# Kernel optimization log

Hardware: AMD Instinct MI355X
Metric: run time of the kernel (lower is better)

Reference implementation:

```python
import jax, jax.numpy as jnp
import numpy as np

EPS = 1e-12

def _dot(x, y):
    return jnp.sum(x * y, axis=-1)

def _safe(x):
    # avoid div-by-zero for degenerate triangles / unused where-branches
    return jnp.where(jnp.abs(x) < EPS, EPS, x)

def _closest_point_on_tri(p, a, b, c):
    """Ericson real-time-collision-detection closest point on triangle.
    p: [B,Q,1,3]; a,b,c: [B,1,F,3]. Returns [B,Q,F,3]."""
    ab = b - a
    ac = c - a
    ap = p - a
    d1 = _dot(ab, ap)
    d2 = _dot(ac, ap)
    bp = p - b
    d3 = _dot(ab, bp)
    d4 = _dot(ac, bp)
    cp = p - c
    d5 = _dot(ab, cp)
    d6 = _dot(ac, cp)
    vc = d1 * d4 - d3 * d2
    vb = d5 * d2 - d1 * d6
    va = d3 * d6 - d5 * d4
    # candidate points (all computed densely, selected by masks)
    t_ab = (d1 / _safe(d1 - d3))[..., None]
    t_ac = (d2 / _safe(d2 - d6))[..., None]
    t_bc = ((d4 - d3) / _safe((d4 - d3) + (d5 - d6)))[..., None]
    denom = _safe(va + vb + vc)
    v = (vb / denom)[..., None]
    w = (vc / denom)[..., None]
    res = a + ab * v + ac * w  # face interior
    cond_bc = ((va <= 0) & ((d4 - d3) >= 0) & ((d5 - d6) >= 0))[..., None]
    cond_ac = ((vb <= 0) & (d2 >= 0) & (d6 <= 0))[..., None]
    cond_c = ((d6 >= 0) & (d5 <= d6))[..., None]
    cond_ab = ((vc <= 0) & (d1 >= 0) & (d3 <= 0))[..., None]
    cond_b = ((d3 >= 0) & (d4 <= d3))[..., None]
    cond_a = ((d1 <= 0) & (d2 <= 0))[..., None]
    res = jnp.where(cond_bc, b + (c - b) * t_bc, res)
    res = jnp.where(cond_ac, a + ac * t_ac, res)
    res = jnp.where(cond_c, c, res)
    res = jnp.where(cond_ab, a + ab * t_ab, res)
    res = jnp.where(cond_b, b, res)
    res = jnp.where(cond_a, a, res)
    return res

def setup_inputs() -> dict:
    key = jax.random.key(0)
    k1, k2, k3 = jax.random.split(key, 3)
    B, nQ, nV, nF = 1, 8192, 1024, 2048
    vertices = jax.random.normal(k1, (B, nV, 3), dtype=jnp.float32)
    query = jax.random.normal(k2, (B, nQ, 3), dtype=jnp.float32)
    faces = jax.random.randint(k3, (nF, 3), 0, nV, dtype=jnp.int32)
    return {"faces": faces, "vertices": vertices, "query": query}

def reference(faces, vertices, query):
    # gather triangle vertices: [B, F, 3(verts), 3(xyz)]
    tri = vertices[:, faces, :]
    a = tri[:, :, 0][:, None]  # [B,1,F,3]
    b = tri[:, :, 1][:, None]
    c = tri[:, :, 2][:, None]
    p = query[:, :, None, :]   # [B,Q,1,3]
    cp = _closest_point_on_tri(p, a, b, c)        # [B,Q,F,3]
    d2 = jnp.sum((p - cp) ** 2, axis=-1)          # [B,Q,F]
    idx = jnp.argmin(d2, axis=-1)                 # [B,Q]
    B_, Q_ = idx.shape
    cp_best = jnp.take_along_axis(
        cp, jnp.broadcast_to(idx[:, :, None, None], (B_, Q_, 1, 3)), axis=2
    )[:, :, 0]                                    # [B,Q,3]
    d2_best = jnp.take_along_axis(d2, idx[:, :, None], axis=2)[:, :, 0]
    # face normals for sign (outside if along normal), per-face then gathered
    n = jnp.cross(tri[:, :, 1] - tri[:, :, 0], tri[:, :, 2] - tri[:, :, 0])  # [B,F,3]
    n_best = jnp.take_along_axis(n, jnp.broadcast_to(idx[:, :, None], (B_, Q_, 3)) % n.shape[1] * 0 + idx[:, :, None], axis=1)  # [B,Q,3]
    sign = jnp.where(jnp.sum((query - cp_best) * n_best, axis=-1) >= 0, 1.0, -1.0)
    sdist = sign * jnp.sqrt(jnp.maximum(d2_best, 0.0))
    phi = jnp.concatenate([cp_best, sdist[..., None]], axis=-1)  # [B,Q,4]
    return phi
```

## Files before the change

kernel.cpp:

```cpp
#include <hip/hip_runtime.h>
#include <stdint.h>


#define QPB 256
#define FC  64
#define RECF 20

__device__ __forceinline__ float safe32(float x) {
    return (fabsf(x) < 1e-12f) ? 1e-12f : x;
}

__device__ __forceinline__ float cp32(
    float px, float py, float pz, const float4* __restrict__ rec,
    float& rx, float& ry, float& rz)
{
#pragma clang fp contract(off)
    float4 r0 = rec[0], r1 = rec[1], r2 = rec[2], r3 = rec[3], r4 = rec[4];
    float ax = r0.x, ay = r0.y, az = r0.z, bx = r0.w;
    float by = r1.x, bz = r1.y, cx = r1.z, cy = r1.w;
    float cz = r2.x, abx = r2.y, aby = r2.z, abz = r2.w;
    float acx = r3.x, acy = r3.y, acz = r3.z, cbx = r3.w;
    float cby = r4.x, cbz = r4.y;

    float apx = px - ax, apy = py - ay, apz = pz - az;
    float bpx = px - bx, bpy = py - by, bpz = pz - bz;
    float qpx = px - cx, qpy = py - cy, qpz = pz - cz;

    float d1 = ((abx * apx) + (aby * apy)) + (abz * apz);
    float d2 = ((acx * apx) + (acy * apy)) + (acz * apz);
    float d3 = ((abx * bpx) + (aby * bpy)) + (abz * bpz);
    float d4 = ((acx * bpx) + (acy * bpy)) + (acz * bpz);
    float d5 = ((abx * qpx) + (aby * qpy)) + (abz * qpz);
    float d6 = ((acx * qpx) + (acy * qpy)) + (acz * qpz);

    float vc = (d1 * d4) - (d3 * d2);
    float vb = (d5 * d2) - (d1 * d6);
    float va = (d3 * d6) - (d5 * d4);
    float e1 = d4 - d3;
    float e2 = d5 - d6;

    bool ca  = (d1 <= 0.0f) && (d2 <= 0.0f);
    bool cb_ = (d3 >= 0.0f) && (d4 <= d3);
    bool cab = (vc <= 0.0f) && (d1 >= 0.0f) && (d3 <= 0.0f);
    bool cc  = (d6 >= 0.0f) && (d5 <= d6);
    bool cac = (vb <= 0.0f) && (d2 >= 0.0f) && (d6 <= 0.0f);
    bool cbc = (va <= 0.0f) && (e1 >= 0.0f) && (e2 >= 0.0f);

    bool tk  = ca;
    bool m_b  = cb_ && !tk;  tk = tk || cb_;
    bool m_ab = cab && !tk;  tk = tk || cab;
    bool m_c  = cc  && !tk;  tk = tk || cc;
    bool m_ac = cac && !tk;  tk = tk || cac;
    bool m_bc = cbc && !tk;  tk = tk || cbc;
    bool m_in = !tk;

    float denom_raw = (va + vb) + vc;
    float num1 = m_ab ? d1 : m_ac ? d2 : m_bc ? e1 : m_in ? vb : 0.0f;
    float den1_raw = m_ab ? (d1 - d3) : m_ac ? (d2 - d6)
                   : m_bc ? (e1 + e2) : m_in ? denom_raw : 1.0f;
    float den1  = safe32(den1_raw);
    float denom = safe32(denom_raw);
    float num2  = m_in ? vc : 0.0f;
    float q1 = num1 / den1;
    float q2 = num2 / denom;

    bool sel_b = m_b || m_bc;
    float basx = m_c ? cx : sel_b ? bx : ax;
    float basy = m_c ? cy : sel_b ? by : ay;
    float basz = m_c ? cz : sel_b ? bz : az;

    bool s_ab = m_ab || m_in;
    float t1x = m_bc ? cbx : m_ac ? acx : s_ab ? abx : 0.0f;
    float t1y = m_bc ? cby : m_ac ? acy : s_ab ? aby : 0.0f;
    float t1z = m_bc ? cbz : m_ac ? acz : s_ab ? abz : 0.0f;

    float t2x = m_in ? acx : 0.0f;
    float t2y = m_in ? acy : 0.0f;
    float t2z = m_in ? acz : 0.0f;

    rx = (basx + (t1x * q1)) + (t2x * q2);
    ry = (basy + (t1y * q1)) + (t2y * q2);
    rz = (basz + (t1z * q1)) + (t2z * q2);

    float dx = px - rx, dy = py - ry, dz = pz - rz;
    return ((dx * dx) + (dy * dy)) + (dz * dz);
}

__global__ void k_prep(const int* __restrict__ faces, const float* __restrict__ verts,
                       float* __restrict__ tris, unsigned long long* __restrict__ keys,
                       int nF, int nQ)
{
#pragma clang fp contract(off)
    int i = blockIdx.x * 256 + threadIdx.x;
    if (i < nQ) keys[i] = 0xffffffffffffffffULL;
    if (i < nF) {
        int i0 = faces[i * 3 + 0], i1 = faces[i * 3 + 1], i2 = faces[i * 3 + 2];
        float ax = verts[i0 * 3], ay = verts[i0 * 3 + 1], az = verts[i0 * 3 + 2];
        float bx = verts[i1 * 3], by = verts[i1 * 3 + 1], bz = verts[i1 * 3 + 2];
        float cx = verts[i2 * 3], cy = verts[i2 * 3 + 1], cz = verts[i2 * 3 + 2];
        float* t = &tris[i * RECF];
        t[0]  = ax; t[1]  = ay; t[2]  = az; t[3]  = bx;
        t[4]  = by; t[5]  = bz; t[6]  = cx; t[7]  = cy;
        t[8]  = cz;
        t[9]  = bx - ax; t[10] = by - ay; t[11] = bz - az;
        t[12] = cx - ax; t[13] = cy - ay; t[14] = cz - az;
        t[15] = cx - bx; t[16] = cy - by; t[17] = cz - bz;
        t[18] = 0.0f; t[19] = 0.0f;
    }
}

__global__ __launch_bounds__(QPB) void k_main(
    const float* __restrict__ tris, const float* __restrict__ query,
    unsigned long long* __restrict__ keys, int nF, int nQ)
{
    __shared__ float4 s4[FC * (RECF / 4)];
    const int fbase = blockIdx.y * FC;
    const int nf = min(FC, nF - fbase);
    const int tid = threadIdx.x;

    {
        const float4* src = (const float4*)&tris[(size_t)fbase * RECF];
        for (int i = tid; i < nf * (RECF / 4); i += QPB) s4[i] = src[i];
    }
    __syncthreads();

    const int q = blockIdx.x * QPB + tid;
    if (q >= nQ) return;
    const float px = query[q * 3], py = query[q * 3 + 1], pz = query[q * 3 + 2];

    float best = 3.402823466e38f;
    int bidx = 0x7fffffff;
    for (int f = 0; f < nf; ++f) {
        float rx, ry, rz;
        float d2 = cp32(px, py, pz, &s4[f * (RECF / 4)], rx, ry, rz);
        if (d2 < best) { best = d2; bidx = fbase + f; }
    }
    unsigned long long key =
        ((unsigned long long)__float_as_uint(best) << 32) | (unsigned)bidx;
    atomicMin(&keys[q], key);
}

__global__ void k_final(const float* __restrict__ tris, const float* __restrict__ query,
                        const unsigned long long* __restrict__ keys,
                        float* __restrict__ out, int nQ)
{
#pragma clang fp contract(off)
    int q = blockIdx.x * 256 + threadIdx.x;
    if (q >= nQ) return;
    unsigned long long key = keys[q];
    unsigned idx = (unsigned)(key & 0xffffffffu);
    float best_d2 = __uint_as_float((unsigned)(key >> 32));

    const float px = query[q * 3], py = query[q * 3 + 1], pz = query[q * 3 + 2];
    const float4* rec = (const float4*)&tris[(size_t)idx * RECF];
    float rx, ry, rz;
    cp32(px, py, pz, rec, rx, ry, rz);

    float4 r2 = rec[2], r3 = rec[3];
    float abx = r2.y, aby = r2.z, abz = r2.w;
    float acx = r3.x, acy = r3.y, acz = r3.z;
    float nx = (aby * acz) - (abz * acy);
    float ny = (abz * acx) - (abx * acz);
    float nz = (abx * acy) - (aby * acx);

    float dx = px - rx, dy = py - ry, dz = pz - rz;
    float sdot = ((dx * nx) + (dy * ny)) + (dz * nz);
    float sgn = (sdot >= 0.0f) ? 1.0f : -1.0f;
    float sdist = sgn * __fsqrt_rn(fmaxf(best_d2, 0.0f));

    out[q * 4 + 0] = rx;
    out[q * 4 + 1] = ry;
    out[q * 4 + 2] = rz;
    out[q * 4 + 3] = sdist;
}

extern "C" void kernel_launch(void* const* d_in, const int* in_sizes, int n_in,
                              void* d_out, int out_size, void* d_ws, size_t ws_size,
                              hipStream_t stream) {
    const int* faces = (const int*)d_in[0];
    const float* verts = (const float*)d_in[1];
    const float* query = (const float*)d_in[2];
    float* out = (float*)d_out;

    const int nF = in_sizes[0] / 3;
    const int nQ = in_sizes[2] / 3;

    unsigned long long* keys = (unsigned long long*)d_ws;
    float* tris = (float*)((char*)d_ws + (size_t)nQ * 8);

    int prep_threads = (nQ > nF ? nQ : nF);
    k_prep<<<(prep_threads + 255) / 256, 256, 0, stream>>>(faces, verts, tris, keys, nF, nQ);

    dim3 grid((nQ + QPB - 1) / QPB, (nF + FC - 1) / FC);
    k_main<<<grid, QPB, 0, stream>>>(tris, query, keys, nF, nQ);

    k_final<<<(nQ + 255) / 256, 256, 0, stream>>>(tris, query, keys, out, nQ);
}
```

Before: 127.2 us.

## Read triangle records directly from global memory instead of LDS staging

Drops the shared-memory staging of triangle records and the block barrier, so each thread reads the records straight from global memory. Every thread in a block reads the same address, so the compiler can turn these into uniform scalar loads. It also halves the faces per block, which doubles the grid and the atomicMin traffic on the keys, and adds a 2x unroll. The risk is that scalar-cache loads with no staging add latency, and that the extra atomics cost more than the removed sync saves.

```diff
diff --git a/kernel.cpp b/kernel.cpp
--- a/kernel.cpp
+++ b/kernel.cpp
@@ -3,7 +3,7 @@
 
 
 #define QPB 256
-#define FC  64
+#define FC  32
 #define RECF 20
 
 __device__ __forceinline__ float safe32(float x) {
@@ -11,16 +11,16 @@
 }
 
 __device__ __forceinline__ float cp32(
-    float px, float py, float pz, const float4* __restrict__ rec,
+    float px, float py, float pz, const float* __restrict__ t,
     float& rx, float& ry, float& rz)
 {
 #pragma clang fp contract(off)
-    float4 r0 = rec[0], r1 = rec[1], r2 = rec[2], r3 = rec[3], r4 = rec[4];
-    float ax = r0.x, ay = r0.y, az = r0.z, bx = r0.w;
-    float by = r1.x, bz = r1.y, cx = r1.z, cy = r1.w;
-    float cz = r2.x, abx = r2.y, aby = r2.z, abz = r2.w;
-    float acx = r3.x, acy = r3.y, acz = r3.z, cbx = r3.w;
-    float cby = r4.x, cbz = r4.y;
+    float ax  = t[0],  ay  = t[1],  az  = t[2];
+    float bx  = t[3],  by  = t[4],  bz  = t[5];
+    float cx  = t[6],  cy  = t[7],  cz  = t[8];
+    float abx = t[9],  aby = t[10], abz = t[11];
+    float acx = t[12], acy = t[13], acz = t[14];
+    float cbx = t[15], cby = t[16], cbz = t[17];
 
     float apx = px - ax, apy = py - ay, apz = pz - az;
     float bpx = px - bx, bpy = py - by, bpz = pz - bz;
@@ -113,26 +113,20 @@
     const float* __restrict__ tris, const float* __restrict__ query,
     unsigned long long* __restrict__ keys, int nF, int nQ)
 {
-    __shared__ float4 s4[FC * (RECF / 4)];
     const int fbase = blockIdx.y * FC;
     const int nf = min(FC, nF - fbase);
-    const int tid = threadIdx.x;
 
-    {
-        const float4* src = (const float4*)&tris[(size_t)fbase * RECF];
-        for (int i = tid; i < nf * (RECF / 4); i += QPB) s4[i] = src[i];
-    }
-    __syncthreads();
-
-    const int q = blockIdx.x * QPB + tid;
+    const int q = blockIdx.x * QPB + threadIdx.x;
     if (q >= nQ) return;
     const float px = query[q * 3], py = query[q * 3 + 1], pz = query[q * 3 + 2];
 
     float best = 3.402823466e38f;
     int bidx = 0x7fffffff;
+#pragma unroll 2
     for (int f = 0; f < nf; ++f) {
         float rx, ry, rz;
-        float d2 = cp32(px, py, pz, &s4[f * (RECF / 4)], rx, ry, rz);
+        float d2 = cp32(px, py, pz, &tris[(size_t)(fbase + f) * RECF],
+                        rx, ry, rz);
         if (d2 < best) { best = d2; bidx = fbase + f; }
     }
     unsigned long long key =
@@ -152,13 +146,12 @@
     float best_d2 = __uint_as_float((unsigned)(key >> 32));
 
     const float px = query[q * 3], py = query[q * 3 + 1], pz = query[q * 3 + 2];
-    const float4* rec = (const float4*)&tris[(size_t)idx * RECF];
+    const float* t = &tris[(size_t)idx * RECF];
     float rx, ry, rz;
-    cp32(px, py, pz, rec, rx, ry, rz);
+    cp32(px, py, pz, t, rx, ry, rz);
 
-    float4 r2 = rec[2], r3 = rec[3];
-    float abx = r2.y, aby = r2.z, abz = r2.w;
-    float acx = r3.x, acy = r3.y, acz = r3.z;
+    float abx = t[9],  aby = t[10], abz = t[11];
+    float acx = t[12], acy = t[13], acz = t[14];
     float nx = (aby * acz) - (abz * acy);
     float ny = (abz * acx) - (abx * acz);
     float nz = (abx * acy) - (aby * acx);
```

Measured after the change: 126.6 us. Within noise of the previous version (-0.5%).
